# Kernel optimization log

Hardware: AMD Instinct MI355X
Metric: run time of the kernel (lower is better)

The kernel has to match this reference:

```python
import jax, jax.numpy as jnp
import numpy as np

N_NODES = 100000
N_EDGES = 1600000
IN = 128
OUT = 32
HEADS = 4
NEG_SLOPE = 0.2


def setup_inputs() -> dict:
    key = jax.random.key(0)
    ks = jax.random.split(key, 6)
    x = jax.random.normal(ks[0], (N_NODES, IN), dtype=jnp.float32)
    row = jax.random.randint(ks[1], (N_EDGES,), 0, N_NODES, dtype=jnp.int32)
    col = jax.random.randint(ks[2], (N_EDGES,), 0, N_NODES, dtype=jnp.int32)
    W = jax.random.normal(ks[3], (OUT * HEADS, IN), dtype=jnp.float32) * (1.0 / np.sqrt(IN))
    b = jnp.zeros((OUT * HEADS,), dtype=jnp.float32)
    a_l = jax.random.normal(ks[4], (1, OUT, HEADS), dtype=jnp.float32) * 0.1
    a_r = jax.random.normal(ks[5], (1, OUT, HEADS), dtype=jnp.float32) * 0.1
    return {"x": x, "row": row, "col": col, "W": W, "b": b, "a_l": a_l, "a_r": a_r}


def reference(x, row, col, W, b, a_l, a_r):
    N = x.shape[0]
    # Z: [N, OUT, HEADS] (row-major view of [N, OUT*HEADS], matching torch .view)
    Z = (x @ W.T + b).reshape(N, OUT, HEADS)
    e_l = jnp.sum(Z * a_l, axis=1)  # [N, HEADS]
    e_r = jnp.sum(Z * a_r, axis=1)  # [N, HEADS]
    e = e_l[row] + e_r[col]         # [E, HEADS]
    e = jnp.where(e > 0, e, NEG_SLOPE * e)  # LeakyReLU
    # segment softmax over edges grouped by destination (row)
    m = jax.ops.segment_max(e, row, num_segments=N)      # [N, HEADS]
    ex = jnp.exp(e - m[row])                              # [E, HEADS]
    denom = jax.ops.segment_sum(ex, row, num_segments=N)  # [N, HEADS]
    alpha = ex / denom[row]                               # [E, HEADS]
    # bspmm: out[i,:,h] = sum_{(i,j) in E} alpha[e,h] * Z[j,:,h]
    out = jax.ops.segment_sum(alpha[:, None, :] * Z[col], row, num_segments=N)
    return out
```

## Files before the change

### kernel.cpp

```cpp
#include <hip/hip_runtime.h>
#include <hip/hip_bf16.h>
#include <math.h>


typedef __attribute__((ext_vector_type(8))) short bf16x8;
typedef __attribute__((ext_vector_type(4))) float f32x4;

__device__ __forceinline__ ushort f2bf(float f) {
  __hip_bfloat16 h = __float2bfloat16(f);
  return __builtin_bit_cast(ushort, h);
}
__device__ __forceinline__ float bf2f(ushort u) {
  unsigned v = ((unsigned)u) << 16;
  return __builtin_bit_cast(float, v);
}

__global__ __launch_bounds__(256) void prep_w(
    const float* __restrict__ W, ushort* __restrict__ Wh,
    ushort* __restrict__ Wl) {
  int i = blockIdx.x * 256 + threadIdx.x;
  float w = W[i];
  ushort hb = f2bf(w);
  Wh[i] = hb;
  Wl[i] = f2bf(w - bf2f(hb));
}

__global__ __launch_bounds__(512, 4) void gemm_z(
    const float* __restrict__ x, const ushort* __restrict__ Wh,
    const ushort* __restrict__ Wl, const float* __restrict__ bias,
    ushort* __restrict__ Zh, int N) {
  __shared__ __align__(16) ushort smem[16384];
  ushort* xh = smem;
  ushort* xl = smem + 8192;
  ushort* zs = smem;
  const int t = threadIdx.x;
  const int lane = t & 63;
  const int wv = t >> 6;
  const int row0 = blockIdx.x * 64;
  const int l15 = lane & 15, l4 = lane >> 4;
  const int ch = wv * 16 + l15;

  bf16x8 Bh[4], Bl[4];
#pragma unroll
  for (int kf = 0; kf < 4; ++kf) {
    int off = ch * 128 + kf * 32 + l4 * 8;
    Bh[kf] = *(const bf16x8*)&Wh[off];
    Bl[kf] = *(const bf16x8*)&Wl[off];
  }

#pragma unroll
  for (int i = 0; i < 4; ++i) {
    int f4 = i * 512 + t;
    int r = f4 >> 5;
    int k = (f4 & 31) * 4;
    int gr = row0 + r;
    float4 v = make_float4(0.f, 0.f, 0.f, 0.f);
    if (gr < N) v = ((const float4*)x)[(size_t)gr * 32 + (f4 & 31)];
    float vf[4] = {v.x, v.y, v.z, v.w};
    ushort hs[4], ls[4];
#pragma unroll
    for (int j = 0; j < 4; ++j) {
      hs[j] = f2bf(vf[j]);
      ls[j] = f2bf(vf[j] - bf2f(hs[j]));
    }
    int idx = r * 128 + (k ^ ((r & 7) << 3));
    uint2 hv, lv;
    hv.x = hs[0] | ((unsigned)hs[1] << 16);
    hv.y = hs[2] | ((unsigned)hs[3] << 16);
    lv.x = ls[0] | ((unsigned)ls[1] << 16);
    lv.y = ls[2] | ((unsigned)ls[3] << 16);
    *(uint2*)&xh[idx] = hv;
    *(uint2*)&xl[idx] = lv;
  }
  __syncthreads();

  f32x4 acc[4];
#pragma unroll
  for (int rt = 0; rt < 4; ++rt) acc[rt] = (f32x4){0.f, 0.f, 0.f, 0.f};

#pragma unroll
  for (int kf = 0; kf < 4; ++kf) {
#pragma unroll
    for (int rt = 0; rt < 4; ++rt) {
      int r = rt * 16 + l15;
      int idx = r * 128 + ((kf * 32 + l4 * 8) ^ ((r & 7) << 3));
      bf16x8 ah = *(const bf16x8*)&xh[idx];
      bf16x8 al = *(const bf16x8*)&xl[idx];
      acc[rt] = __builtin_amdgcn_mfma_f32_16x16x32_bf16(ah, Bh[kf], acc[rt], 0, 0, 0);
      acc[rt] = __builtin_amdgcn_mfma_f32_16x16x32_bf16(al, Bh[kf], acc[rt], 0, 0, 0);
      acc[rt] = __builtin_amdgcn_mfma_f32_16x16x32_bf16(ah, Bl[kf], acc[rt], 0, 0, 0);
    }
  }
  __syncthreads();

  {
    float bv = bias[ch];
    int o = ch >> 2, h = ch & 3;
    int s = (o & 15) * 8 + h * 2 + (o >> 4);
#pragma unroll
    for (int rt = 0; rt < 4; ++rt) {
#pragma unroll
      for (int j = 0; j < 4; ++j) {
        int r = rt * 16 + l4 * 4 + j;
        zs[r * 132 + s] = f2bf(acc[rt][j] + bv);
      }
    }
  }
  __syncthreads();
  {
    int r = t >> 3;
    int c = t & 7;
    int gr = row0 + r;
    if (gr < N) {
      uint4 v0 = *(const uint4*)&zs[r * 132 + c * 16];
      uint4 v1 = *(const uint4*)&zs[r * 132 + c * 16 + 8];
      *(uint4*)&Zh[(size_t)gr * 128 + c * 16] = v0;
      *(uint4*)&Zh[(size_t)gr * 128 + c * 16 + 8] = v1;
    }
  }
}

__global__ __launch_bounds__(256) void deg_cnt(
    const int* __restrict__ row, int* __restrict__ deg,
    int* __restrict__ rank, int E) {
  int e = blockIdx.x * 256 + threadIdx.x;
  if (e < E) rank[e] = atomicAdd(&deg[row[e]], 1);
}

__global__ __launch_bounds__(256) void node_scan(
    const ushort* __restrict__ Zh, const float* __restrict__ a_l,
    const float* __restrict__ a_r, float* __restrict__ el,
    float* __restrict__ er, int N4,
    const int* __restrict__ deg, int* __restrict__ basev,
    int* __restrict__ bsum, int N, int G1) {
  __shared__ float sal[128], sar[128];
  __shared__ int ss[256];
  int t = threadIdx.x;

  if ((int)blockIdx.x < G1) {
    if (t < 128) { sal[t] = a_l[t]; sar[t] = a_r[t]; }
    __syncthreads();
    int idx = blockIdx.x * 256 + t;
    if (idx >= N4) return;
    int n = idx >> 2, h = idx & 3;
    const unsigned* zp = (const unsigned*)Zh + (unsigned)n * 64 + h;
    float sl = 0.f, sr = 0.f;
#pragma unroll
    for (int o = 0; o < 16; ++o) {
      unsigned zz = zp[o * 4];
      float zlo = bf2f((ushort)(zz & 0xffff));
      float zhi = bf2f((ushort)(zz >> 16));
      int c = (o << 2) + h;
      sl += zlo * sal[c] + zhi * sal[c + 64];
      sr += zlo * sar[c] + zhi * sar[c + 64];
    }
    el[idx] = sl;
    er[idx] = sr;
  } else {
    int bid = (int)blockIdx.x - G1;
    int i = bid * 256 + t;
    int v = (i < N) ? deg[i] : 0;
    ss[t] = v;
    __syncthreads();
#pragma unroll
    for (int off = 1; off < 256; off <<= 1) {
      int u = (t >= off) ? ss[t - off] : 0;
      __syncthreads();
      ss[t] += u;
      __syncthreads();
    }
    if (i < N) basev[i] = ss[t] - v;
    if (t == 255) bsum[bid] = ss[255];
  }
}

__global__ __launch_bounds__(512) void scan2(int* __restrict__ bsum, int NB) {
  __shared__ int s[512];
  int v = (threadIdx.x < NB) ? bsum[threadIdx.x] : 0;
  s[threadIdx.x] = v;
  __syncthreads();
#pragma unroll
  for (int off = 1; off < 512; off <<= 1) {
    int t = (threadIdx.x >= off) ? s[threadIdx.x - off] : 0;
    __syncthreads();
    s[threadIdx.x] += t;
    __syncthreads();
  }
  if (threadIdx.x < NB) bsum[threadIdx.x] = s[threadIdx.x] - v;
}

__global__ __launch_bounds__(256) void fill(
    const int* __restrict__ row, const int* __restrict__ col,
    const int* __restrict__ rank, const int* __restrict__ base,
    const int* __restrict__ bsum, int* __restrict__ sorted_col, int E) {
  int e = blockIdx.x * 256 + threadIdx.x;
  if (e < E) {
    int r = row[e];
    sorted_col[base[r] + bsum[r >> 8] + rank[e]] = col[e];
  }
}

__global__ __launch_bounds__(256) void gather(
    const int* __restrict__ base, const int* __restrict__ bsum,
    const int* __restrict__ deg, const int* __restrict__ sorted_col,
    const float* __restrict__ el, const float* __restrict__ er,
    const ushort* __restrict__ Zh, float* __restrict__ out, int N) {
  int t = threadIdx.x;
  int lane = t & 63;
  int n = blockIdx.x * 4 + (t >> 6);
  if (n >= N) return;
  int h = lane & 3;
  int jj = lane >> 2;
  int s = base[n] + bsum[n >> 8];
  int d = deg[n];
  int end = s + d;
  float elv = el[((unsigned)n << 2) + h];
  float acc0 = 0.f, acc1 = 0.f, sumA = 0.f;
  const unsigned* Zh32 = (const unsigned*)Zh;
  const unsigned zlane = (unsigned)lane;
  const int bpb = (lane & 3) << 2;

  for (int p = s; p < end; p += 16) {
    int cnt = end - p;
    int cl6 = 0;
    float xv = 0.f;
    if (jj < cnt) {
      int cl = sorted_col[p + jj];
      float e = elv + er[((unsigned)cl << 2) + h];
      e = fmaxf(e, 0.2f * e);
      xv = __expf(e);
      cl6 = cl << 6;
    }
    sumA += xv;
    float xvb[16];
    unsigned addr[16];
#pragma unroll
    for (int q = 0; q < 16; ++q) {
      int a = bpb + (q << 4);
      xvb[q] = __builtin_bit_cast(float,
          __builtin_amdgcn_ds_bpermute(a, __builtin_bit_cast(int, xv)));
      addr[q] = (unsigned)__builtin_amdgcn_ds_bpermute(a, cl6) + zlane;
    }
    unsigned zz[16];
#pragma unroll
    for (int q = 0; q < 16; ++q) zz[q] = Zh32[addr[q]];
#pragma unroll
    for (int q = 0; q < 16; ++q) {
      acc0 = fmaf(xvb[q], __builtin_bit_cast(float, zz[q] << 16), acc0);
      acc1 = fmaf(xvb[q], __builtin_bit_cast(float, zz[q] & 0xffff0000u), acc1);
    }
  }
  float sum = sumA;
  sum += __shfl_xor(sum, 4, 64);
  sum += __shfl_xor(sum, 8, 64);
  sum += __shfl_xor(sum, 16, 64);
  sum += __shfl_xor(sum, 32, 64);
  float inv = (d > 0) ? 1.0f / sum : 0.f;
  unsigned ob = ((unsigned)n << 7) + zlane;
  __builtin_nontemporal_store(acc0 * inv, &out[ob]);
  __builtin_nontemporal_store(acc1 * inv, &out[ob + 64]);
}

extern "C" void kernel_launch(void* const* d_in, const int* in_sizes, int n_in,
                              void* d_out, int out_size, void* d_ws, size_t ws_size,
                              hipStream_t stream) {
  const float* x   = (const float*)d_in[0];
  const int*   row = (const int*)d_in[1];
  const int*   col = (const int*)d_in[2];
  const float* W   = (const float*)d_in[3];
  const float* b   = (const float*)d_in[4];
  const float* a_l = (const float*)d_in[5];
  const float* a_r = (const float*)d_in[6];
  float* out = (float*)d_out;

  const int N = in_sizes[0] / 128;
  const int E = in_sizes[1];
  const int NB = (N + 255) / 256;

  char* w = (char*)d_ws;
  ushort* Zh       = (ushort*)w;             w += (size_t)N * 128 * 2;
  int*   sorted_col= (int*)w;                w += (size_t)E * 4;
  int*   rank      = (int*)w;                w += (size_t)E * 4;
  float* el        = (float*)w;              w += (size_t)N * 4 * 4;
  float* er        = (float*)w;              w += (size_t)N * 4 * 4;
  int*   deg       = (int*)w;                w += (size_t)N * 4;
  int*   base      = (int*)w;                w += (size_t)N * 4;
  int*   bsum      = (int*)w;                w += 512 * 4;
  ushort* Wh       = (ushort*)w;             w += 16384 * 2;
  ushort* Wl       = (ushort*)w;             w += 16384 * 2;

  hipMemsetAsync(deg, 0, (size_t)N * sizeof(int), stream);

  prep_w<<<64, 256, 0, stream>>>(W, Wh, Wl);
  deg_cnt<<<(E + 255) / 256, 256, 0, stream>>>(row, deg, rank, E);
  gemm_z<<<(N + 63) / 64, 512, 0, stream>>>(x, Wh, Wl, b, Zh, N);

  const int G1n = (N * 4 + 255) / 256;
  node_scan<<<G1n + NB, 256, 0, stream>>>(Zh, a_l, a_r, el, er, N * 4,
                                          deg, base, bsum, N, G1n);
  scan2<<<1, 512, 0, stream>>>(bsum, NB);
  fill<<<(E + 255) / 256, 256, 0, stream>>>(row, col, rank, base, bsum,
                                            sorted_col, E);
  gather<<<(N + 3) / 4, 256, 0, stream>>>(base, bsum, deg, sorted_col, el, er,
                                          Zh, out, N);
}
```

Before: 211.2 us.

## Fuse degree count, GEMM and attention-score computation; drop low-x split term

The W bf16 split is merged with zeroing of the degree array, replacing the memset. The GEMM kernel now also runs the edge degree-count atomics as extra blocks and computes el/er from the shared-memory Z tile, which removes the separate node pass that re-read Zh. It also widens the tile to 128 rows and drops the x-low-part MFMA term, cutting MFMA work and LDS traffic at the cost of some precision in Z. Fewer launches and less global reread are the intended savings.

```diff
diff --git a/kernel.cpp b/kernel.cpp
--- a/kernel.cpp
+++ b/kernel.cpp
@@ -15,30 +15,43 @@
   return __builtin_bit_cast(float, v);
 }
 
-__global__ __launch_bounds__(256) void prep_w(
+__global__ __launch_bounds__(512) void prep0(
     const float* __restrict__ W, ushort* __restrict__ Wh,
-    ushort* __restrict__ Wl) {
-  int i = blockIdx.x * 256 + threadIdx.x;
-  float w = W[i];
-  ushort hb = f2bf(w);
-  Wh[i] = hb;
-  Wl[i] = f2bf(w - bf2f(hb));
-}
-
-__global__ __launch_bounds__(512, 4) void gemm_z(
+    ushort* __restrict__ Wl, int* __restrict__ deg, int N) {
+  int i = blockIdx.x * 512 + threadIdx.x;
+  if (i < 16384) {
+    float w = W[i];
+    ushort hb = f2bf(w);
+    Wh[i] = hb;
+    Wl[i] = f2bf(w - bf2f(hb));
+  }
+  if (i < N) deg[i] = 0;
+}
+
+__global__ __launch_bounds__(512, 4) void gemm_deg(
     const float* __restrict__ x, const ushort* __restrict__ Wh,
     const ushort* __restrict__ Wl, const float* __restrict__ bias,
-    ushort* __restrict__ Zh, int N) {
-  __shared__ __align__(16) ushort smem[16384];
-  ushort* xh = smem;
-  ushort* xl = smem + 8192;
-  ushort* zs = smem;
+    const float* __restrict__ a_l, const float* __restrict__ a_r,
+    ushort* __restrict__ Zh, float* __restrict__ el, float* __restrict__ er,
+    int N, const int* __restrict__ row, int* __restrict__ deg,
+    int* __restrict__ rank, int E, int G1) {
+  __shared__ __align__(16) ushort smem[16896];
+  __shared__ float sal[128], sar[128];
+
+  if ((int)blockIdx.x >= G1) {
+    int e = ((int)blockIdx.x - G1) * 512 + threadIdx.x;
+    if (e < E) rank[e] = atomicAdd(&deg[row[e]], 1);
+    return;
+  }
+
   const int t = threadIdx.x;
   const int lane = t & 63;
   const int wv = t >> 6;
-  const int row0 = blockIdx.x * 64;
+  const int row0 = blockIdx.x * 128;
   const int l15 = lane & 15, l4 = lane >> 4;
   const int ch = wv * 16 + l15;
+
+  if (t < 128) { sal[t] = a_l[t]; sar[t] = a_r[t]; }
 
   bf16x8 Bh[4], Bl[4];
 #pragma unroll
@@ -48,57 +61,47 @@
     Bl[kf] = *(const bf16x8*)&Wl[off];
   }
 
-#pragma unroll
-  for (int i = 0; i < 4; ++i) {
+  ushort* xh = smem;
+#pragma unroll
+  for (int i = 0; i < 8; ++i) {
     int f4 = i * 512 + t;
     int r = f4 >> 5;
     int k = (f4 & 31) * 4;
     int gr = row0 + r;
     float4 v = make_float4(0.f, 0.f, 0.f, 0.f);
     if (gr < N) v = ((const float4*)x)[(size_t)gr * 32 + (f4 & 31)];
-    float vf[4] = {v.x, v.y, v.z, v.w};
-    ushort hs[4], ls[4];
-#pragma unroll
-    for (int j = 0; j < 4; ++j) {
-      hs[j] = f2bf(vf[j]);
-      ls[j] = f2bf(vf[j] - bf2f(hs[j]));
-    }
     int idx = r * 128 + (k ^ ((r & 7) << 3));
-    uint2 hv, lv;
-    hv.x = hs[0] | ((unsigned)hs[1] << 16);
-    hv.y = hs[2] | ((unsigned)hs[3] << 16);
-    lv.x = ls[0] | ((unsigned)ls[1] << 16);
-    lv.y = ls[2] | ((unsigned)ls[3] << 16);
+    uint2 hv;
+    hv.x = f2bf(v.x) | ((unsigned)f2bf(v.y) << 16);
+    hv.y = f2bf(v.z) | ((unsigned)f2bf(v.w) << 16);
     *(uint2*)&xh[idx] = hv;
-    *(uint2*)&xl[idx] = lv;
-  }
-  __syncthreads();
-
-  f32x4 acc[4];
-#pragma unroll
-  for (int rt = 0; rt < 4; ++rt) acc[rt] = (f32x4){0.f, 0.f, 0.f, 0.f};
+  }
+  __syncthreads();
+
+  f32x4 acc[8];
+#pragma unroll
+  for (int rt = 0; rt < 8; ++rt) acc[rt] = (f32x4){0.f, 0.f, 0.f, 0.f};
 
 #pragma unroll
   for (int kf = 0; kf < 4; ++kf) {
 #pragma unroll
-    for (int rt = 0; rt < 4; ++rt) {
+    for (int rt = 0; rt < 8; ++rt) {
       int r = rt * 16 + l15;
       int idx = r * 128 + ((kf * 32 + l4 * 8) ^ ((r & 7) << 3));
       bf16x8 ah = *(const bf16x8*)&xh[idx];
-      bf16x8 al = *(const bf16x8*)&xl[idx];
       acc[rt] = __builtin_amdgcn_mfma_f32_16x16x32_bf16(ah, Bh[kf], acc[rt], 0, 0, 0);
-      acc[rt] = __builtin_amdgcn_mfma_f32_16x16x32_bf16(al, Bh[kf], acc[rt], 0, 0, 0);
       acc[rt] = __builtin_amdgcn_mfma_f32_16x16x32_bf16(ah, Bl[kf], acc[rt], 0, 0, 0);
     }
   }
   __syncthreads();
 
+  ushort* zs = smem;
   {
     float bv = bias[ch];
     int o = ch >> 2, h = ch & 3;
     int s = (o & 15) * 8 + h * 2 + (o >> 4);
 #pragma unroll
-    for (int rt = 0; rt < 4; ++rt) {
+    for (int rt = 0; rt < 8; ++rt) {
 #pragma unroll
       for (int j = 0; j < 4; ++j) {
         int r = rt * 16 + l4 * 4 + j;
@@ -107,71 +110,50 @@
     }
   }
   __syncthreads();
+
   {
-    int r = t >> 3;
-    int c = t & 7;
+    int r = t >> 2;
+    int h = t & 3;
     int gr = row0 + r;
     if (gr < N) {
-      uint4 v0 = *(const uint4*)&zs[r * 132 + c * 16];
-      uint4 v1 = *(const uint4*)&zs[r * 132 + c * 16 + 8];
-      *(uint4*)&Zh[(size_t)gr * 128 + c * 16] = v0;
-      *(uint4*)&Zh[(size_t)gr * 128 + c * 16 + 8] = v1;
-    }
-  }
-}
-
-__global__ __launch_bounds__(256) void deg_cnt(
-    const int* __restrict__ row, int* __restrict__ deg,
-    int* __restrict__ rank, int E) {
-  int e = blockIdx.x * 256 + threadIdx.x;
-  if (e < E) rank[e] = atomicAdd(&deg[row[e]], 1);
-}
-
-__global__ __launch_bounds__(256) void node_scan(
-    const ushort* __restrict__ Zh, const float* __restrict__ a_l,
-    const float* __restrict__ a_r, float* __restrict__ el,
-    float* __restrict__ er, int N4,
-    const int* __restrict__ deg, int* __restrict__ basev,
-    int* __restrict__ bsum, int N, int G1) {
-  __shared__ float sal[128], sar[128];
-  __shared__ int ss[256];
-  int t = threadIdx.x;
-
-  if ((int)blockIdx.x < G1) {
-    if (t < 128) { sal[t] = a_l[t]; sar[t] = a_r[t]; }
-    __syncthreads();
-    int idx = blockIdx.x * 256 + t;
-    if (idx >= N4) return;
-    int n = idx >> 2, h = idx & 3;
-    const unsigned* zp = (const unsigned*)Zh + (unsigned)n * 64 + h;
-    float sl = 0.f, sr = 0.f;
-#pragma unroll
-    for (int o = 0; o < 16; ++o) {
-      unsigned zz = zp[o * 4];
-      float zlo = bf2f((ushort)(zz & 0xffff));
-      float zhi = bf2f((ushort)(zz >> 16));
-      int c = (o << 2) + h;
-      sl += zlo * sal[c] + zhi * sal[c + 64];
-      sr += zlo * sar[c] + zhi * sar[c + 64];
-    }
-    el[idx] = sl;
-    er[idx] = sr;
-  } else {
-    int bid = (int)blockIdx.x - G1;
-    int i = bid * 256 + t;
-    int v = (i < N) ? deg[i] : 0;
-    ss[t] = v;
-    __syncthreads();
-#pragma unroll
-    for (int off = 1; off < 256; off <<= 1) {
-      int u = (t >= off) ? ss[t - off] : 0;
-      __syncthreads();
-      ss[t] += u;
-      __syncthreads();
-    }
-    if (i < N) basev[i] = ss[t] - v;
-    if (t == 255) bsum[bid] = ss[255];
-  }
+#pragma unroll
+      for (int q = 0; q < 4; ++q) {
+        uint4 v = *(const uint4*)&zs[r * 132 + h * 32 + q * 8];
+        *(uint4*)&Zh[(size_t)gr * 128 + h * 32 + q * 8] = v;
+      }
+      float sl = 0.f, sr = 0.f;
+#pragma unroll
+      for (int op = 0; op < 16; ++op) {
+        unsigned zz = *(const unsigned*)&zs[r * 132 + op * 8 + h * 2];
+        float zlo = bf2f((ushort)(zz & 0xffff));
+        float zhi = bf2f((ushort)(zz >> 16));
+        int c = (op << 2) + h;
+        sl += zlo * sal[c] + zhi * sal[c + 64];
+        sr += zlo * sar[c] + zhi * sar[c + 64];
+      }
+      el[(unsigned)gr * 4 + h] = sl;
+      er[(unsigned)gr * 4 + h] = sr;
+    }
+  }
+}
+
+__global__ __launch_bounds__(256) void scan1(
+    const int* __restrict__ deg, int* __restrict__ base,
+    int* __restrict__ bsum, int N) {
+  __shared__ int s[256];
+  int i = blockIdx.x * 256 + threadIdx.x;
+  int v = (i < N) ? deg[i] : 0;
+  s[threadIdx.x] = v;
+  __syncthreads();
+#pragma unroll
+  for (int off = 1; off < 256; off <<= 1) {
+    int t = (threadIdx.x >= off) ? s[threadIdx.x - off] : 0;
+    __syncthreads();
+    s[threadIdx.x] += t;
+    __syncthreads();
+  }
+  if (i < N) base[i] = s[threadIdx.x] - v;
+  if (threadIdx.x == 255) bsum[blockIdx.x] = s[255];
 }
 
 __global__ __launch_bounds__(512) void scan2(int* __restrict__ bsum, int NB) {
@@ -289,15 +271,15 @@
   ushort* Wh       = (ushort*)w;             w += 16384 * 2;
   ushort* Wl       = (ushort*)w;             w += 16384 * 2;
 
-  hipMemsetAsync(deg, 0, (size_t)N * sizeof(int), stream);
-
-  prep_w<<<64, 256, 0, stream>>>(W, Wh, Wl);
-  deg_cnt<<<(E + 255) / 256, 256, 0, stream>>>(row, deg, rank, E);
-  gemm_z<<<(N + 63) / 64, 512, 0, stream>>>(x, Wh, Wl, b, Zh, N);
-
-  const int G1n = (N * 4 + 255) / 256;
-  node_scan<<<G1n + NB, 256, 0, stream>>>(Zh, a_l, a_r, el, er, N * 4,
-                                          deg, base, bsum, N, G1n);
+  const int P0 = (N > 16384 ? N : 16384);
+  prep0<<<(P0 + 511) / 512, 512, 0, stream>>>(W, Wh, Wl, deg, N);
+
+  const int G1 = (N + 127) / 128;
+  const int G2 = (E + 511) / 512;
+  gemm_deg<<<G1 + G2, 512, 0, stream>>>(x, Wh, Wl, b, a_l, a_r, Zh, el, er,
+                                        N, row, deg, rank, E, G1);
+
+  scan1<<<NB, 256, 0, stream>>>(deg, base, bsum, N);
   scan2<<<1, 512, 0, stream>>>(bsum, NB);
   fill<<<(E + 255) / 256, 256, 0, stream>>>(row, col, rank, base, bsum,
                                             sorted_col, E);
```

New measurement: 195.2 us. 7.6% less time.
